# Optimization experiments

Measured on AMD Instinct MI355X. Metric: run time of the kernel, lower is better.

## Reference

```python
import jax, jax.numpy as jnp
import numpy as np

N_NODES = 100000
LN_EPS = 1e-5
NEG_SLOPE = 0.2


def setup_inputs() -> dict:
    key = jax.random.key(0)
    ks = jax.random.split(key, 6)
    N, E, NIN, EDIM, NOUT, H = N_NODES, 1600000, 64, 32, 128, 4
    x = jax.random.normal(ks[0], (N, NIN), dtype=jnp.float32)
    edge_index = jax.random.randint(ks[1], (2, E), 0, N, dtype=jnp.int64)
    edge_attr = jax.random.normal(ks[2], (E, EDIM), dtype=jnp.float32)
    # xavier-uniform linear weights (torch layout: [out, in])
    def xavier(k, fan_out, fan_in):
        lim = float(np.sqrt(6.0 / (fan_in + fan_out)))
        return jax.random.uniform(k, (fan_out, fan_in), jnp.float32, -lim, lim)
    W_msg = xavier(ks[3], NOUT, NIN + EDIM)          # (128, 96)
    W_att = xavier(ks[4], H, 2 * NIN + EDIM)         # (4, 160)
    bias = jnp.zeros((NOUT,), jnp.float32)
    ln_gamma = jnp.ones((NOUT,), jnp.float32)
    ln_beta = jnp.zeros((NOUT,), jnp.float32)
    return {"x": x, "edge_index": edge_index, "edge_attr": edge_attr,
            "W_msg": W_msg, "W_att": W_att, "bias": bias,
            "ln_gamma": ln_gamma, "ln_beta": ln_beta}


def reference(x, edge_index, edge_attr, W_msg, W_att, bias, ln_gamma, ln_beta):
    N = x.shape[0]
    H = W_att.shape[0]
    src, dst = edge_index[0], edge_index[1]
    xs = x[src]                                       # (E, node_in) gather
    xd = x[dst]                                       # (E, node_in) gather
    # message: W_msg @ [h_u ; x_uv]
    msg_in = jnp.concatenate([xs, edge_attr], axis=-1)            # (E, 96)
    msgs = msg_in @ W_msg.T                                        # (E, out_dim)
    msgs = msgs.reshape(-1, H, W_msg.shape[0] // H)                # (E, H, D)
    # attention logits: LeakyReLU(W_att @ [h_u ; h_v ; x_uv])
    att_in = jnp.concatenate([xs, xd, edge_attr], axis=-1)         # (E, 160)
    logits = att_in @ W_att.T                                      # (E, H)
    logits = jax.nn.leaky_relu(logits, NEG_SLOPE)
    # per-destination-node sparse softmax
    seg_max = jax.ops.segment_max(logits, dst, num_segments=N)     # (N, H)
    exp_l = jnp.exp(logits - seg_max[dst])                         # (E, H)
    seg_sum = jax.ops.segment_sum(exp_l, dst, num_segments=N)      # (N, H)
    att = exp_l / (seg_sum[dst] + 1e-9)                            # (E, H)
    # weighted scatter-add aggregation
    weighted = msgs * att[..., None]                               # (E, H, D)
    out = jax.ops.segment_sum(weighted, dst, num_segments=N)       # (N, H, D)
    out = out.reshape(N, -1) + bias                                # concat heads
    # layer norm over feature dim
    mu = out.mean(axis=-1, keepdims=True)
    var = out.var(axis=-1, keepdims=True)
    out = (out - mu) * jax.lax.rsqrt(var + LN_EPS) * ln_gamma + ln_beta
    return out
```

## Files before the change

kernel.cpp:

```cpp
#include <hip/hip_runtime.h>
#include <hip/hip_bf16.h>

typedef __attribute__((ext_vector_type(8))) short short8;
typedef __attribute__((ext_vector_type(4))) float f32x4;

__device__ __forceinline__ unsigned short fbf(float f) {
  union { float f; unsigned u; } v; v.f = f;
  unsigned r = v.u + 0x7fffu + ((v.u >> 16) & 1u);
  return (unsigned short)(r >> 16);
}
__device__ __forceinline__ unsigned pk2(float a, float b) {
  return (unsigned)fbf(a) | ((unsigned)fbf(b) << 16);
}
__device__ __forceinline__ float ubf(unsigned hi) {
  union { unsigned u; float f; } v; v.u = hi << 16; return v.f;
}
__device__ __forceinline__ float ubf_lo(unsigned u) {
  union { unsigned u; float f; } v; v.u = u << 16; return v.f;
}
__device__ __forceinline__ float ubf_hi(unsigned u) {
  union { unsigned u; float f; } v; v.u = u & 0xffff0000u; return v.f;
}
__device__ __forceinline__ float dot4(float4 a, float4 b) {
  return fmaf(a.x, b.x, fmaf(a.y, b.y, fmaf(a.z, b.z, a.w * b.w)));
}

__launch_bounds__(256)
__global__ void k_phase1(const float* __restrict__ x, const float* __restrict__ W_att,
                         const int* __restrict__ edst, int E,
                         float4* __restrict__ A_s, float4* __restrict__ A_d,
                         unsigned* __restrict__ xb32, int* __restrict__ deg, int N) {
  __shared__ float4 s_wa[160];
  if (threadIdx.x < 160) s_wa[threadIdx.x] = ((const float4*)W_att)[threadIdx.x];
  for (int i = blockIdx.x * blockDim.x + threadIdx.x; i < E; i += gridDim.x * blockDim.x)
    atomicAdd(&deg[edst[i]], 1);
  __syncthreads();
  for (int v = blockIdx.x * blockDim.x + threadIdx.x; v < N; v += gridDim.x * blockDim.x) {
    const float4* xp = (const float4*)&x[v * 64];
    float4 xq[16];
    #pragma unroll
    for (int k = 0; k < 16; k++) xq[k] = xp[k];
    float as[4] = {}, ad[4] = {};
    #pragma unroll
    for (int h = 0; h < 4; h++) {
      #pragma unroll
      for (int k = 0; k < 16; k++) {
        as[h] += dot4(s_wa[h * 40 + k], xq[k]);
        ad[h] += dot4(s_wa[h * 40 + 16 + k], xq[k]);
      }
    }
    A_s[v] = make_float4(as[0], as[1], as[2], as[3]);
    A_d[v] = make_float4(ad[0], ad[1], ad[2], ad[3]);
    #pragma unroll
    for (int k = 0; k < 16; k++) {
      xb32[v * 32 + 2 * k]     = pk2(xq[k].x, xq[k].y);
      xb32[v * 32 + 2 * k + 1] = pk2(xq[k].z, xq[k].w);
    }
  }
}

__global__ void k_scan1(const int* __restrict__ deg, int N, int* __restrict__ part,
                        int* __restrict__ bsum) {
  __shared__ int tmp[1024];
  int tid = threadIdx.x;
  int i = blockIdx.x * 1024 + tid;
  int dv = (i < N) ? deg[i] : 0;
  int v = (dv + 7) & ~7;
  tmp[tid] = v;
  __syncthreads();
  for (int ofs = 1; ofs < 1024; ofs <<= 1) {
    int t = (tid >= ofs) ? tmp[tid - ofs] : 0;
    __syncthreads();
    tmp[tid] += t;
    __syncthreads();
  }
  if (i < N) part[i] = tmp[tid] - v;
  if (tid == 1023) bsum[blockIdx.x] = tmp[tid];
}

__global__ void k_scan2(int* __restrict__ part, const int* __restrict__ bsum,
                        const int* __restrict__ deg, int N, int* __restrict__ cursor,
                        int4* __restrict__ csrp) {
  __shared__ int sbase;
  if (threadIdx.x == 0) {
    int b = 0;
    for (int j = 0; j < (int)blockIdx.x; j++) b += bsum[j];
    sbase = b;
  }
  __syncthreads();
  int i = blockIdx.x * 1024 + threadIdx.x;
  if (i < N) {
    const int o = part[i] + sbase;
    part[i] = o;
    cursor[i] = o;
    const int d = deg[i];
    const int pe = o + ((d + 7) & ~7);
    const int4 z = make_int4(0, 0, 0, 0);
    for (int s = o + d; s < pe; s++) csrp[s] = z;
    if (i == N - 1) part[N] = pe;
  }
}

__launch_bounds__(256)
__global__ void k_fillP(const int* __restrict__ esrc, const int* __restrict__ edst, int E,
                        const float* __restrict__ ea, const float4* __restrict__ A_s,
                        const float4* __restrict__ A_d, const float* __restrict__ W_att,
                        int* __restrict__ cursor, int4* __restrict__ csrp) {
  __shared__ float4 s_we[32];
  if (threadIdx.x < 32) {
    int h = threadIdx.x >> 3, k4 = threadIdx.x & 7;
    const float* p = &W_att[h * 160 + 128 + k4 * 4];
    s_we[threadIdx.x] = make_float4(p[0], p[1], p[2], p[3]);
  }
  __syncthreads();
  const int stride = gridDim.x * blockDim.x;
  for (int e1 = blockIdx.x * blockDim.x + threadIdx.x; e1 < E; e1 += 2 * stride) {
    const int e2 = e1 + stride;
    const bool has2 = (e2 < E);
    const int e2c = has2 ? e2 : e1;
    const int s1 = esrc[e1], d1 = edst[e1];
    const int s2 = esrc[e2c], d2 = edst[e2c];
    const int slot1 = atomicAdd(&cursor[d1], 1);
    const int slot2 = has2 ? atomicAdd(&cursor[d2], 1) : 0;
    const float4 as1 = A_s[s1], ad1 = A_d[d1];
    const float4 as2 = A_s[s2], ad2 = A_d[d2];
    float lgA0 = as1.x + ad1.x, lgA1 = as1.y + ad1.y;
    float lgA2 = as1.z + ad1.z, lgA3 = as1.w + ad1.w;
    float lgB0 = as2.x + ad2.x, lgB1 = as2.y + ad2.y;
    float lgB2 = as2.z + ad2.z, lgB3 = as2.w + ad2.w;
    const float4* ep1 = (const float4*)&ea[(unsigned)e1 * 32u];
    const float4* ep2 = (const float4*)&ea[(unsigned)e2c * 32u];
    #pragma unroll
    for (int k = 0; k < 8; k++) {
      const float4 q1 = ep1[k];
      const float4 q2 = ep2[k];
      lgA0 += dot4(s_we[0 * 8 + k], q1); lgB0 += dot4(s_we[0 * 8 + k], q2);
      lgA1 += dot4(s_we[1 * 8 + k], q1); lgB1 += dot4(s_we[1 * 8 + k], q2);
      lgA2 += dot4(s_we[2 * 8 + k], q1); lgB2 += dot4(s_we[2 * 8 + k], q2);
      lgA3 += dot4(s_we[3 * 8 + k], q1); lgB3 += dot4(s_we[3 * 8 + k], q2);
    }
    lgA0 = fmaxf(lgA0, 0.2f * lgA0); lgA1 = fmaxf(lgA1, 0.2f * lgA1);
    lgA2 = fmaxf(lgA2, 0.2f * lgA2); lgA3 = fmaxf(lgA3, 0.2f * lgA3);
    lgB0 = fmaxf(lgB0, 0.2f * lgB0); lgB1 = fmaxf(lgB1, 0.2f * lgB1);
    lgB2 = fmaxf(lgB2, 0.2f * lgB2); lgB3 = fmaxf(lgB3, 0.2f * lgB3);
    csrp[slot1] = make_int4(s1, e1,
                            (int)pk2(__expf(lgA0), __expf(lgA1)),
                            (int)pk2(__expf(lgA2), __expf(lgA3)));
    if (has2)
      csrp[slot2] = make_int4(s2, e2,
                              (int)pk2(__expf(lgB0), __expf(lgB1)),
                              (int)pk2(__expf(lgB2), __expf(lgB3)));
  }
}

__launch_bounds__(256)
__global__ void k_aggP(const unsigned short* __restrict__ xb, const float* __restrict__ ea,
                       const int4* __restrict__ csrp, const int* __restrict__ offsets,
                       unsigned short* __restrict__ agg, float* __restrict__ denom, int N) {
  __shared__ int4 s_ids[4][32];
  const int lane = threadIdx.x & 63;
  const int wvb = threadIdx.x >> 6;
  const int wv = (blockIdx.x * blockDim.x + threadIdx.x) >> 6;
  const int nw = (gridDim.x * blockDim.x) >> 6;
  const int l32 = lane & 31;
  const bool hi = lane >= 32;

  for (int v0 = wv; v0 < N; v0 += nw) {
    const int vv = __builtin_amdgcn_readfirstlane(v0);
    const int sstart = __builtin_amdgcn_readfirstlane(offsets[vv]);
    const int send = __builtin_amdgcn_readfirstlane(offsets[vv + 1]);
    const int ng = (send - sstart) >> 3;
    const int nq = (ng + 3) >> 2;

    float ax0 = 0, ax1 = 0, ax2 = 0, ax3 = 0;
    float ae0 = 0, ae1 = 0, ae2 = 0, ae3 = 0;
    float dn0 = 0, dn1 = 0, dn2 = 0, dn3 = 0;

    for (int q = 0; q < nq; q++) {
      {
        int4 q_ = csrp[sstart + q * 32 + l32];
        if (lane < 32) s_ids[wvb][l32] = q_;
      }
      const int nsc = min(4, ng - q * 4);
      float ev[4][8];
      unsigned short qv[4][8];
      #pragma unroll
      for (int sc = 0; sc < 4; sc++) {
        if (sc < nsc) {
          #pragma unroll
          for (int p = 0; p < 8; p++) {
            const int4 t_ = s_ids[wvb][sc * 8 + p];
            qv[sc][p] = xb[(unsigned)(t_.x << 6) + lane];
            ev[sc][p] = ea[(unsigned)(t_.y << 5) + l32];
          }
        }
      }
      #pragma unroll
      for (int sc = 0; sc < 4; sc++) {
        if (sc < nsc) {
          #pragma unroll
          for (int p = 0; p < 8; p++) {
            const int4 t_ = s_ids[wvb][sc * 8 + p];
            const float a0_ = ubf_lo((unsigned)t_.z);
            const float a1_ = ubf_hi((unsigned)t_.z);
            const float a2_ = ubf_lo((unsigned)t_.w);
            const float a3_ = ubf_hi((unsigned)t_.w);
            const float xf = ubf((unsigned)qv[sc][p]);
            const float evp = ev[sc][p];
            ax0 = fmaf(a0_, xf, ax0); ax1 = fmaf(a1_, xf, ax1);
            ax2 = fmaf(a2_, xf, ax2); ax3 = fmaf(a3_, xf, ax3);
            ae0 = fmaf(a0_, evp, ae0); ae1 = fmaf(a1_, evp, ae1);
            ae2 = fmaf(a2_, evp, ae2); ae3 = fmaf(a3_, evp, ae3);
            dn0 += a0_; dn1 += a1_; dn2 += a2_; dn3 += a3_;
          }
        }
      }
    }

    const unsigned base = (unsigned)v0 * 384u;
    agg[base + lane]        = fbf(ax0);
    agg[base + 96 + lane]   = fbf(ax1);
    agg[base + 192 + lane]  = fbf(ax2);
    agg[base + 288 + lane]  = fbf(ax3);
    const int hA = hi ? 2 : 0;
    agg[base + hA * 96 + 64 + l32]       = fbf(hi ? ae2 : ae0);
    agg[base + (hA + 1) * 96 + 64 + l32] = fbf(hi ? ae3 : ae1);
    if (lane == 0) ((float4*)denom)[v0] = make_float4(dn0, dn1, dn2, dn3);
  }
}

__launch_bounds__(128)
__global__ void k_out(const unsigned short* __restrict__ agg, const float* __restrict__ W_msg,
                      const float* __restrict__ denom, const float* __restrict__ bias,
                      const float* __restrict__ gamma, const float* __restrict__ beta,
                      float* __restrict__ out, int N, int T) {
  __shared__ float s_den[64];
  __shared__ float s_sum[2][16], s_sq[2][16];
  const int f = threadIdx.x;
  const int w = f >> 6;
  const int l = f & 63;
  const int c16 = l & 15;
  const int rg = l >> 4;

  short8 wb[2][2][3];
  float biasv[2][2], gv[2][2], bv[2][2];
  #pragma unroll
  for (int hh = 0; hh < 2; hh++) {
    const int head = 2 * w + hh;
    #pragma unroll
    for (int ct = 0; ct < 2; ct++) {
      const int q = head * 32 + ct * 16 + c16;
      biasv[hh][ct] = bias[q]; gv[hh][ct] = gamma[q]; bv[hh][ct] = beta[q];
      #pragma unroll
      for (int kk = 0; kk < 3; kk++) {
        const float* p = &W_msg[q * 96 + kk * 32 + rg * 8];
        short8 s;
        #pragma unroll
        for (int i = 0; i < 8; i++) s[i] = (short)fbf(p[i]);
        wb[hh][ct][kk] = s;
      }
    }
  }

  for (int t = blockIdx.x; t < T; t += gridDim.x) {
    const int n0 = t * 16;
    if (f < 64) s_den[f] = denom[min(n0 + (f >> 2), N - 1) * 4 + (f & 3)];
    __syncthreads();

    f32x4 c[2][2] = {{{0.f,0.f,0.f,0.f},{0.f,0.f,0.f,0.f}},
                     {{0.f,0.f,0.f,0.f},{0.f,0.f,0.f,0.f}}};
    const int nA = min(n0 + c16, N - 1);
    #pragma unroll
    for (int hh = 0; hh < 2; hh++) {
      const int head = 2 * w + hh;
      #pragma unroll
      for (int kk = 0; kk < 3; kk++) {
        short8 a = *(const short8*)&agg[nA * 384 + head * 96 + kk * 32 + rg * 8];
        c[hh][0] = __builtin_amdgcn_mfma_f32_16x16x32_bf16(a, wb[hh][0][kk], c[hh][0], 0, 0, 0);
        c[hh][1] = __builtin_amdgcn_mfma_f32_16x16x32_bf16(a, wb[hh][1][kk], c[hh][1], 0, 0, 0);
      }
    }

    float val[2][2][4];
    #pragma unroll
    for (int hh = 0; hh < 2; hh++)
      #pragma unroll
      for (int ct = 0; ct < 2; ct++)
        #pragma unroll
        for (int r = 0; r < 4; r++) {
          const float d = s_den[(rg * 4 + r) * 4 + (2 * w + hh)] + 1e-9f;
          val[hh][ct][r] = c[hh][ct][r] / d + biasv[hh][ct];
        }

    float sr[4], qr[4];
    #pragma unroll
    for (int r = 0; r < 4; r++) {
      float s = 0.f, q2 = 0.f;
      #pragma unroll
      for (int hh = 0; hh < 2; hh++)
        #pragma unroll
        for (int ct = 0; ct < 2; ct++) { s += val[hh][ct][r]; q2 = fmaf(val[hh][ct][r], val[hh][ct][r], q2); }
      #pragma unroll
      for (int m = 1; m <= 8; m <<= 1) { s += __shfl_xor(s, m, 64); q2 += __shfl_xor(q2, m, 64); }
      sr[r] = s; qr[r] = q2;
    }
    if (c16 == 0) {
      #pragma unroll
      for (int r = 0; r < 4; r++) { s_sum[w][rg * 4 + r] = sr[r]; s_sq[w][rg * 4 + r] = qr[r]; }
    }
    __syncthreads();

    float mean[4], rstd[4];
    #pragma unroll
    for (int r = 0; r < 4; r++) {
      const int ni = rg * 4 + r;
      mean[r] = (s_sum[0][ni] + s_sum[1][ni]) * (1.f / 128.f);
      const float m2 = (s_sq[0][ni] + s_sq[1][ni]) * (1.f / 128.f);
      rstd[r] = rsqrtf(m2 - mean[r] * mean[r] + 1e-5f);
    }
    #pragma unroll
    for (int hh = 0; hh < 2; hh++)
      #pragma unroll
      for (int ct = 0; ct < 2; ct++)
        #pragma unroll
        for (int r = 0; r < 4; r++) {
          const int n = n0 + rg * 4 + r;
          if (n < N)
            out[n * 128 + (2 * w + hh) * 32 + ct * 16 + c16] =
                (val[hh][ct][r] - mean[r]) * rstd[r] * gv[hh][ct] + bv[hh][ct];
        }
    __syncthreads();
  }
}

extern "C" void kernel_launch(void* const* d_in, const int* in_sizes, int n_in,
                              void* d_out, int out_size, void* d_ws, size_t ws_size,
                              hipStream_t stream) {
  const float* x     = (const float*)d_in[0];
  const int*   ei    = (const int*)d_in[1];
  const float* ea    = (const float*)d_in[2];
  const float* W_msg = (const float*)d_in[3];
  const float* W_att = (const float*)d_in[4];
  const float* bias  = (const float*)d_in[5];
  const float* gamma = (const float*)d_in[6];
  const float* beta  = (const float*)d_in[7];
  float* out = (float*)d_out;

  const int N = in_sizes[0] / 64;
  const int E = in_sizes[1] / 2;
  const int* esrc = ei;
  const int* edst = ei + E;
  const int EP = E + 8 * N + 64;

  char* p = (char*)d_ws;
  int* deg      = (int*)p;            p += (size_t)N * 4;
  int* offsets  = (int*)p;            p += (size_t)(N + 1) * 4;
  int* cursor   = (int*)p;            p += (size_t)N * 4;
  int* bsum     = (int*)p;            p += 2048 * 4;
  int4* csrp    = (int4*)p;           p += (size_t)EP * 16;
  float4* A_s   = (float4*)p;         p += (size_t)N * 16;
  float4* A_d   = (float4*)p;         p += (size_t)N * 16;
  unsigned short* xb = (unsigned short*)p; p += (size_t)N * 64 * 2;
  unsigned short* agg = (unsigned short*)p; p += (size_t)N * 384 * 2;
  float* denom  = (float*)p;

  hipMemsetAsync(deg, 0, (size_t)N * 4, stream);
  const int SB = (N + 1023) / 1024;
  const int T = (N + 15) / 16;

  k_phase1<<<2048, 256, 0, stream>>>(x, W_att, edst, E, A_s, A_d, (unsigned*)xb, deg, N);
  k_scan1<<<SB, 1024, 0, stream>>>(deg, N, offsets, bsum);
  k_scan2<<<SB, 1024, 0, stream>>>(offsets, bsum, deg, N, cursor, csrp);
  k_fillP<<<2048, 256, 0, stream>>>(esrc, edst, E, ea, A_s, A_d, W_att, cursor, csrp);
  k_aggP<<<2048, 256, 0, stream>>>(xb, ea, csrp, offsets, agg, denom, N);
  k_out<<<T, 128, 0, stream>>>(agg, W_msg, denom, bias, gamma, beta, out, N, T);
}
```

Measured before the change: 416.4 us.

## Record per-edge rank in degree pass to remove second atomic cursor pass

The degree-counting atomicAdd now stores its returned value as a per-edge rank. The CSR fill kernel computes each slot as offsets[dst] + rank, so it no longer needs a second round of atomics on a cursor array. The fill loop is also simplified from two edges per thread to one, and loads the edge attributes up front. This adds an E-sized rank array (written once, read once) in exchange for removing 1.6M contended atomics.

```diff
diff --git a/kernel.cpp b/kernel.cpp
--- a/kernel.cpp
+++ b/kernel.cpp
@@ -29,11 +29,12 @@
 __global__ void k_phase1(const float* __restrict__ x, const float* __restrict__ W_att,
                          const int* __restrict__ edst, int E,
                          float4* __restrict__ A_s, float4* __restrict__ A_d,
-                         unsigned* __restrict__ xb32, int* __restrict__ deg, int N) {
+                         unsigned* __restrict__ xb32, int* __restrict__ deg,
+                         int* __restrict__ rank, int N) {
   __shared__ float4 s_wa[160];
   if (threadIdx.x < 160) s_wa[threadIdx.x] = ((const float4*)W_att)[threadIdx.x];
   for (int i = blockIdx.x * blockDim.x + threadIdx.x; i < E; i += gridDim.x * blockDim.x)
-    atomicAdd(&deg[edst[i]], 1);
+    rank[i] = atomicAdd(&deg[edst[i]], 1);
   __syncthreads();
   for (int v = blockIdx.x * blockDim.x + threadIdx.x; v < N; v += gridDim.x * blockDim.x) {
     const float4* xp = (const float4*)&x[v * 64];
@@ -79,8 +80,7 @@
 }
 
 __global__ void k_scan2(int* __restrict__ part, const int* __restrict__ bsum,
-                        const int* __restrict__ deg, int N, int* __restrict__ cursor,
-                        int4* __restrict__ csrp) {
+                        const int* __restrict__ deg, int N, int4* __restrict__ csrp) {
   __shared__ int sbase;
   if (threadIdx.x == 0) {
     int b = 0;
@@ -92,7 +92,6 @@
   if (i < N) {
     const int o = part[i] + sbase;
     part[i] = o;
-    cursor[i] = o;
     const int d = deg[i];
     const int pe = o + ((d + 7) & ~7);
     const int4 z = make_int4(0, 0, 0, 0);
@@ -105,7 +104,8 @@
 __global__ void k_fillP(const int* __restrict__ esrc, const int* __restrict__ edst, int E,
                         const float* __restrict__ ea, const float4* __restrict__ A_s,
                         const float4* __restrict__ A_d, const float* __restrict__ W_att,
-                        int* __restrict__ cursor, int4* __restrict__ csrp) {
+                        const int* __restrict__ offsets, const int* __restrict__ rank,
+                        int4* __restrict__ csrp) {
   __shared__ float4 s_we[32];
   if (threadIdx.x < 32) {
     int h = threadIdx.x >> 3, k4 = threadIdx.x & 7;
@@ -113,43 +113,25 @@
     s_we[threadIdx.x] = make_float4(p[0], p[1], p[2], p[3]);
   }
   __syncthreads();
-  const int stride = gridDim.x * blockDim.x;
-  for (int e1 = blockIdx.x * blockDim.x + threadIdx.x; e1 < E; e1 += 2 * stride) {
-    const int e2 = e1 + stride;
-    const bool has2 = (e2 < E);
-    const int e2c = has2 ? e2 : e1;
-    const int s1 = esrc[e1], d1 = edst[e1];
-    const int s2 = esrc[e2c], d2 = edst[e2c];
-    const int slot1 = atomicAdd(&cursor[d1], 1);
-    const int slot2 = has2 ? atomicAdd(&cursor[d2], 1) : 0;
-    const float4 as1 = A_s[s1], ad1 = A_d[d1];
-    const float4 as2 = A_s[s2], ad2 = A_d[d2];
-    float lgA0 = as1.x + ad1.x, lgA1 = as1.y + ad1.y;
-    float lgA2 = as1.z + ad1.z, lgA3 = as1.w + ad1.w;
-    float lgB0 = as2.x + ad2.x, lgB1 = as2.y + ad2.y;
-    float lgB2 = as2.z + ad2.z, lgB3 = as2.w + ad2.w;
-    const float4* ep1 = (const float4*)&ea[(unsigned)e1 * 32u];
-    const float4* ep2 = (const float4*)&ea[(unsigned)e2c * 32u];
-    #pragma unroll
-    for (int k = 0; k < 8; k++) {
-      const float4 q1 = ep1[k];
-      const float4 q2 = ep2[k];
-      lgA0 += dot4(s_we[0 * 8 + k], q1); lgB0 += dot4(s_we[0 * 8 + k], q2);
-      lgA1 += dot4(s_we[1 * 8 + k], q1); lgB1 += dot4(s_we[1 * 8 + k], q2);
-      lgA2 += dot4(s_we[2 * 8 + k], q1); lgB2 += dot4(s_we[2 * 8 + k], q2);
-      lgA3 += dot4(s_we[3 * 8 + k], q1); lgB3 += dot4(s_we[3 * 8 + k], q2);
-    }
-    lgA0 = fmaxf(lgA0, 0.2f * lgA0); lgA1 = fmaxf(lgA1, 0.2f * lgA1);
-    lgA2 = fmaxf(lgA2, 0.2f * lgA2); lgA3 = fmaxf(lgA3, 0.2f * lgA3);
-    lgB0 = fmaxf(lgB0, 0.2f * lgB0); lgB1 = fmaxf(lgB1, 0.2f * lgB1);
-    lgB2 = fmaxf(lgB2, 0.2f * lgB2); lgB3 = fmaxf(lgB3, 0.2f * lgB3);
-    csrp[slot1] = make_int4(s1, e1,
-                            (int)pk2(__expf(lgA0), __expf(lgA1)),
-                            (int)pk2(__expf(lgA2), __expf(lgA3)));
-    if (has2)
-      csrp[slot2] = make_int4(s2, e2,
-                              (int)pk2(__expf(lgB0), __expf(lgB1)),
-                              (int)pk2(__expf(lgB2), __expf(lgB3)));
+  for (int e = blockIdx.x * blockDim.x + threadIdx.x; e < E; e += gridDim.x * blockDim.x) {
+    const int s = esrc[e], d = edst[e];
+    const int slot = offsets[d] + rank[e];
+    const float4* ep = (const float4*)&ea[(unsigned)e * 32u];
+    float4 eq[8];
+    #pragma unroll
+    for (int k = 0; k < 8; k++) eq[k] = ep[k];
+    const float4 as4 = A_s[s], ad4 = A_d[d];
+    const float base[4] = {as4.x + ad4.x, as4.y + ad4.y, as4.z + ad4.z, as4.w + ad4.w};
+    float av[4];
+    #pragma unroll
+    for (int h = 0; h < 4; h++) {
+      float lg = base[h];
+      #pragma unroll
+      for (int k = 0; k < 8; k++) lg += dot4(s_we[h * 8 + k], eq[k]);
+      lg = fmaxf(lg, 0.2f * lg);
+      av[h] = __expf(lg);
+    }
+    csrp[slot] = make_int4(s, e, (int)pk2(av[0], av[1]), (int)pk2(av[2], av[3]));
   }
 }
 
@@ -355,7 +337,7 @@
   char* p = (char*)d_ws;
   int* deg      = (int*)p;            p += (size_t)N * 4;
   int* offsets  = (int*)p;            p += (size_t)(N + 1) * 4;
-  int* cursor   = (int*)p;            p += (size_t)N * 4;
+  int* rank     = (int*)p;            p += (size_t)E * 4;
   int* bsum     = (int*)p;            p += 2048 * 4;
   int4* csrp    = (int4*)p;           p += (size_t)EP * 16;
   float4* A_s   = (float4*)p;         p += (size_t)N * 16;
@@ -368,10 +350,10 @@
   const int SB = (N + 1023) / 1024;
   const int T = (N + 15) / 16;
 
-  k_phase1<<<2048, 256, 0, stream>>>(x, W_att, edst, E, A_s, A_d, (unsigned*)xb, deg, N);
+  k_phase1<<<2048, 256, 0, stream>>>(x, W_att, edst, E, A_s, A_d, (unsigned*)xb, deg, rank, N);
   k_scan1<<<SB, 1024, 0, stream>>>(deg, N, offsets, bsum);
-  k_scan2<<<SB, 1024, 0, stream>>>(offsets, bsum, deg, N, cursor, csrp);
-  k_fillP<<<2048, 256, 0, stream>>>(esrc, edst, E, ea, A_s, A_d, W_att, cursor, csrp);
+  k_scan2<<<SB, 1024, 0, stream>>>(offsets, bsum, deg, N, csrp);
+  k_fillP<<<2048, 256, 0, stream>>>(esrc, edst, E, ea, A_s, A_d, W_att, offsets, rank, csrp);
   k_aggP<<<2048, 256, 0, stream>>>(xb, ea, csrp, offsets, agg, denom, N);
   k_out<<<T, 128, 0, stream>>>(agg, W_msg, denom, bias, gamma, beta, out, N, T);
 }
```

Result: faster. 393.6 us (-5.5%).
